# Kernel optimization log

Measured on AMD Instinct MI355X. Metric: run time of the kernel, lower is better.

The kernel has to match this reference:

```python
import jax, jax.numpy as jnp
import numpy as np

S, B, D = 2048, 2, 1024
H, HD = 16, 64  # head_num, head_dim
SCALE = 1.0 / (HD ** 0.5)


def setup_inputs() -> dict:
    key = jax.random.key(0)
    ks = jax.random.split(key, 7)
    std = 1.0 / np.sqrt(D)
    return {
        "inputs": jax.random.normal(ks[0], (S, B, D), dtype=jnp.float32),
        "Wkv": jax.random.uniform(ks[1], (D, 2 * H * HD), jnp.float32, -std, std),
        "bkv": jax.random.uniform(ks[2], (2 * H * HD,), jnp.float32, -std, std),
        "Wq": jax.random.uniform(ks[3], (D, H * HD), jnp.float32, -std, std),
        "bq": jax.random.uniform(ks[4], (H * HD,), jnp.float32, -std, std),
        "Wp": jax.random.uniform(ks[5], (H * HD, D), jnp.float32, -std, std),
        "bp": jax.random.uniform(ks[6], (D,), jnp.float32, -std, std),
    }


def reference(inputs, Wkv, bkv, Wq, bq, Wp, bp):
    s, b, _ = inputs.shape
    kv = inputs @ Wkv + bkv                      # [S,B,2*H*HD]
    k, v = jnp.split(kv, 2, axis=-1)
    q = inputs @ Wq + bq                         # [S,B,H*HD]
    k = k.reshape(s, b, H, HD)
    q = q.reshape(s, b, H, HD)
    v = v.reshape(s, b, H, HD)
    # scores: [B,H,S,S]
    attn = jnp.einsum("sbhd,tbhd->bhst", q, k) * SCALE
    attn = jax.nn.softmax(attn, axis=-1)         # dropout is identity in eval
    attn_vec = jnp.einsum("bhst,tbhd->sbhd", attn, v)
    attn_vec = attn_vec.reshape(s, b, H * HD)
    return attn_vec @ Wp + bp                    # [S,B,D]
```

## Files before the change

kernel.cpp:

```cpp
#include <hip/hip_runtime.h>
#include <hip/hip_bf16.h>
#include <stdint.h>


typedef __bf16 bf16_t;
typedef __bf16 bf16x8 __attribute__((ext_vector_type(8)));
typedef __bf16 bf16x4 __attribute__((ext_vector_type(4)));
typedef __bf16 bf16x2 __attribute__((ext_vector_type(2)));
typedef float f32x4 __attribute__((ext_vector_type(4)));
typedef float f32x16 __attribute__((ext_vector_type(16)));
typedef uint32_t u32;

#define S_LEN 2048
#define BATCH 2
#define DMODEL 1024
#define NHEAD 16
#define HDIM 64
#define KVB 64
#define FNT (S_LEN / KVB)
#define Q_SCALE 0.1803368801111204f

__device__ inline void gld16(const void* g, void* l)
{
    __builtin_amdgcn_global_load_lds(
        (const __attribute__((address_space(1))) void*)g,
        (__attribute__((address_space(3))) void*)l, 16, 0, 0);
}

__device__ inline u32 pack2(float a, float b)
{
    union { bf16x2 h; u32 u; } c;
    c.h[0] = (bf16_t)a; c.h[1] = (bf16_t)b;
    return c.u;
}

__global__ __launch_bounds__(256) void xcvt_kernel(
    const float* __restrict__ in, bf16_t* __restrict__ out)
{
    size_t i = ((size_t)blockIdx.x * 256 + threadIdx.x) * 8;
    float4 f0 = *(const float4*)(in + i);
    float4 f1 = *(const float4*)(in + i + 4);
    bf16x8 o;
    o[0] = (bf16_t)f0.x; o[1] = (bf16_t)f0.y; o[2] = (bf16_t)f0.z; o[3] = (bf16_t)f0.w;
    o[4] = (bf16_t)f1.x; o[5] = (bf16_t)f1.y; o[6] = (bf16_t)f1.z; o[7] = (bf16_t)f1.w;
    *(bf16x8*)(out + i) = o;
}

__global__ __launch_bounds__(256) void transpose_convert(
    const float* __restrict__ in, bf16_t* __restrict__ out, int K, int N)
{
    __shared__ float tile[64][65];
    int n0 = blockIdx.x * 64, k0 = blockIdx.y * 64;
    int r = threadIdx.x >> 2;
    int c = (threadIdx.x & 3) * 16;
    const float* src = in + (size_t)(k0 + r) * N + n0 + c;
#pragma unroll
    for (int j = 0; j < 16; j += 4) {
        float4 f = *(const float4*)(src + j);
        tile[r][c + j + 0] = f.x;
        tile[r][c + j + 1] = f.y;
        tile[r][c + j + 2] = f.z;
        tile[r][c + j + 3] = f.w;
    }
    __syncthreads();
    bf16x8 o0, o1;
#pragma unroll
    for (int j = 0; j < 8; ++j) o0[j] = (bf16_t)tile[c + j][r];
#pragma unroll
    for (int j = 0; j < 8; ++j) o1[j] = (bf16_t)tile[c + 8 + j][r];
    bf16_t* dst = out + (size_t)(n0 + r) * K + k0 + c;
    *(bf16x8*)dst = o0;
    *(bf16x8*)(dst + 8) = o1;
}

__global__ __launch_bounds__(256) void gemm_qkv(
    const bf16_t* __restrict__ A, const bf16_t* __restrict__ WT,
    const float* __restrict__ bkv, const float* __restrict__ bq,
    bf16_t* __restrict__ outK, bf16_t* __restrict__ outV,
    bf16_t* __restrict__ outQ)
{
    const int K = 1024;
    __shared__ __align__(16) char AsB[128 * 128];
    __shared__ __align__(16) char BsB[128 * 128];
    int tid = threadIdx.x;
    int wave = tid >> 6, lane = tid & 63;
    int l15 = lane & 15, l4 = lane >> 4;
    int m0 = blockIdx.x * 128, n0 = blockIdx.y * 128;
    int wr = (wave >> 1) * 64, wc = (wave & 1) * 64;

    char* ldsT = (wave < 2) ? AsB : BsB;
    const bf16_t* gbase = (wave < 2) ? A : WT;
    int rbase = (wave & 1) * 64;
    int tile0 = (wave < 2) ? m0 : n0;
    int srow = lane >> 3;
    int kcb = ((lane & 7) << 4) ^ (srow << 4);
    int rx = (l15 & 7) << 4;

    f32x4 acc[4][4] = {};

    for (int k0 = 0; k0 < K; k0 += 64) {
#pragma unroll
        for (int j = 0; j < 8; ++j) {
            const char* g = (const char*)(gbase +
                (size_t)(tile0 + rbase + j * 8 + srow) * K + k0) + kcb;
            gld16(g, ldsT + (rbase + j * 8) * 128);
        }
        __syncthreads();
#pragma unroll
        for (int kk = 0; kk < 2; ++kk) {
            int cb = (kk * 64 + l4 * 16) ^ rx;
            bf16x8 af[4], bfr[4];
#pragma unroll
            for (int i = 0; i < 4; ++i)
                af[i] = *(const bf16x8*)(AsB + (wr + i * 16 + l15) * 128 + cb);
#pragma unroll
            for (int i = 0; i < 4; ++i)
                bfr[i] = *(const bf16x8*)(BsB + (wc + i * 16 + l15) * 128 + cb);
#pragma unroll
            for (int mi = 0; mi < 4; ++mi)
#pragma unroll
                for (int ni = 0; ni < 4; ++ni)
                    acc[mi][ni] = __builtin_amdgcn_mfma_f32_16x16x32_bf16(
                        af[mi], bfr[ni], acc[mi][ni], 0, 0, 0);
        }
        __syncthreads();
    }

#pragma unroll
    for (int mi = 0; mi < 4; ++mi) {
#pragma unroll
        for (int ni = 0; ni < 4; ++ni) {
#pragma unroll
            for (int e = 0; e < 4; ++e) {
                int gm = m0 + wr + mi * 16 + l4 * 4 + e;
                int gn = n0 + wc + ni * 16 + l15;
                float bsel = (gn < 2048) ? bkv[gn] : bq[gn - 2048];
                float v = acc[mi][ni][e] + bsel;
                int s = gm >> 1, b = gm & 1;
                int nn = gn & 1023;
                int h = nn >> 6, d = nn & 63;
                size_t idx = ((size_t)((b << 4) + h) * S_LEN + s) * HDIM + d;
                if (gn < 1024)
                    outK[idx] = (bf16_t)v;
                else if (gn < 2048)
                    outV[idx] = (bf16_t)v;
                else
                    outQ[idx] = (bf16_t)(v * Q_SCALE);
            }
        }
    }
}

__global__ __launch_bounds__(256) void gemm_out_kernel(
    const bf16_t* __restrict__ A, const bf16_t* __restrict__ WT,
    const float* __restrict__ bias, float* __restrict__ outF)
{
    const int K = 1024, N = 1024;
    __shared__ __align__(16) char AsB[64 * 128];
    __shared__ __align__(16) char BsB[128 * 128];
    int tid = threadIdx.x, wave = tid >> 6, lane = tid & 63;
    int l15 = lane & 15, l4 = lane >> 4;
    int m0 = blockIdx.x * 64, n0 = blockIdx.y * 128;
    int wc = wave * 32;
    int srow = lane >> 3;
    int kcb = ((lane & 7) << 4) ^ (srow << 4);
    int rx = (l15 & 7) << 4;

    f32x4 acc[4][2] = {};

    for (int k0 = 0; k0 < K; k0 += 64) {
#pragma unroll
        for (int j = 0; j < 6; ++j) {
            int slot = wave * 6 + j;
            const bf16_t* g;
            char* l;
            if (slot < 8) {
                g = A + (size_t)(m0 + slot * 8 + srow) * K + k0;
                l = AsB + slot * 1024;
            } else {
                g = WT + (size_t)(n0 + (slot - 8) * 8 + srow) * K + k0;
                l = BsB + (slot - 8) * 1024;
            }
            gld16((const char*)g + kcb, l);
        }
        __syncthreads();
#pragma unroll
        for (int kk = 0; kk < 2; ++kk) {
            int cb = (kk * 64 + l4 * 16) ^ rx;
            bf16x8 af[4], bfr[2];
#pragma unroll
            for (int i = 0; i < 4; ++i)
                af[i] = *(const bf16x8*)(AsB + (i * 16 + l15) * 128 + cb);
#pragma unroll
            for (int i = 0; i < 2; ++i)
                bfr[i] = *(const bf16x8*)(BsB + (wc + i * 16 + l15) * 128 + cb);
#pragma unroll
            for (int mi = 0; mi < 4; ++mi)
#pragma unroll
                for (int ni = 0; ni < 2; ++ni)
                    acc[mi][ni] = __builtin_amdgcn_mfma_f32_16x16x32_bf16(
                        af[mi], bfr[ni], acc[mi][ni], 0, 0, 0);
        }
        __syncthreads();
    }

#pragma unroll
    for (int mi = 0; mi < 4; ++mi)
#pragma unroll
        for (int ni = 0; ni < 2; ++ni)
#pragma unroll
            for (int e = 0; e < 4; ++e) {
                int gm = m0 + mi * 16 + l4 * 4 + e;
                int gn = n0 + wc + ni * 16 + l15;
                outF[(size_t)gm * N + gn] = acc[mi][ni][e] + bias[gn];
            }
}

__global__ __launch_bounds__(256) void flash_kernel(
    const bf16_t* __restrict__ Qb, const bf16_t* __restrict__ Kb,
    const bf16_t* __restrict__ Vb, bf16_t* __restrict__ AVb)
{
    __shared__ __align__(16) char lds[34816];
    char* KsB = lds;
    bf16_t* VtB = (bf16_t*)(lds + 16384);

    int bh = blockIdx.y;
    int tid = threadIdx.x, wave = tid >> 6, lane = tid & 63;
    int l31 = lane & 31, hi = lane >> 5;

    const bf16_t* Qp = Qb + (size_t)bh * S_LEN * HDIM;
    const bf16_t* Kp = Kb + (size_t)bh * S_LEN * HDIM;
    const bf16_t* Vp = Vb + (size_t)bh * S_LEN * HDIM;

    int q0 = blockIdx.x * 128 + wave * 32;

    bf16x8 qf[4];
#pragma unroll
    for (int dc = 0; dc < 4; ++dc)
        qf[dc] = *(const bf16x8*)(Qp + (size_t)(q0 + l31) * HDIM + dc * 16 + hi * 8);

    f32x16 acc0 = {}, acc1 = {};
    float l_run = 0.f;

    int krow = lane >> 3;
    int kcb = ((lane & 7) << 4) ^ (krow << 4);
    int vd = (tid >> 4) * 4;
    int vt = (tid & 15) * 2;
    bf16x4 vreg[2][2];
    int swz = (l31 & 7) << 4;

#define STAGE_K(it, buf)                                                       \
    {                                                                          \
        _Pragma("unroll")                                                      \
        for (int j = 0; j < 2; ++j) {                                          \
            int t = wave * 16 + j * 8 + krow;                                  \
            const char* g = (const char*)Kp +                                  \
                ((size_t)((it) * KVB + t) * HDIM) * 2 + kcb;                   \
            gld16(g, KsB + (buf) * 8192 + (wave * 16 + j * 8) * 128);          \
        }                                                                      \
    }
#define LOAD_V(it)                                                             \
    {                                                                          \
        const bf16_t* vb = Vp + (size_t)((it) * KVB + vt) * HDIM + vd;         \
        vreg[0][0] = *(const bf16x4*)vb;                                       \
        vreg[0][1] = *(const bf16x4*)(vb + HDIM);                              \
        vreg[1][0] = *(const bf16x4*)(vb + 32 * HDIM);                         \
        vreg[1][1] = *(const bf16x4*)(vb + 33 * HDIM);                         \
    }
#define WRITE_V(buf)                                                           \
    {                                                                          \
        bf16_t* vtb = VtB + (buf) * 4608;                                      \
        _Pragma("unroll")                                                      \
        for (int p = 0; p < 2; ++p) {                                          \
            _Pragma("unroll")                                                  \
            for (int j = 0; j < 4; ++j) {                                      \
                bf16x2 w;                                                      \
                w[0] = vreg[p][0][j];                                          \
                w[1] = vreg[p][1][j];                                          \
                *(bf16x2*)&vtb[(vd + j) * 72 + vt + 32 * p] = w;               \
            }                                                                  \
        }                                                                      \
    }

    STAGE_K(0, 0);
    LOAD_V(0);
    WRITE_V(0);
    __syncthreads();

    for (int it = 0; it < FNT; ++it) {
        int cur = it & 1;
        if (it + 1 < FNT) {
            STAGE_K(it + 1, cur ^ 1);
            LOAD_V(it + 1);
        }

        f32x16 s0 = {}, s1 = {};
        __builtin_amdgcn_s_setprio(1);
#pragma unroll
        for (int dc = 0; dc < 4; ++dc) {
            bf16x8 k0 = *(const bf16x8*)(KsB + cur * 8192 + l31 * 128 +
                                         ((dc * 32 + hi * 16) ^ swz));
            bf16x8 k1 = *(const bf16x8*)(KsB + cur * 8192 + (32 + l31) * 128 +
                                         ((dc * 32 + hi * 16) ^ swz));
            s0 = __builtin_amdgcn_mfma_f32_32x32x16_bf16(k0, qf[dc], s0, 0, 0, 0);
            s1 = __builtin_amdgcn_mfma_f32_32x32x16_bf16(k1, qf[dc], s1, 0, 0, 0);
        }
        __builtin_amdgcn_s_setprio(0);

#pragma unroll
        for (int r = 0; r < 16; ++r) s0[r] = __builtin_amdgcn_exp2f(s0[r]);
#pragma unroll
        for (int r = 0; r < 16; ++r) s1[r] = __builtin_amdgcn_exp2f(s1[r]);
        float a8[8];
#pragma unroll
        for (int r = 0; r < 8; ++r)
            a8[r] = (s0[r] + s0[r + 8]) + (s1[r] + s1[r + 8]);
        float rs = ((a8[0] + a8[1]) + (a8[2] + a8[3])) +
                   ((a8[4] + a8[5]) + (a8[6] + a8[7]));
        rs += __shfl_xor(rs, 32);
        l_run += rs;

        __builtin_amdgcn_s_setprio(1);
#pragma unroll
        for (int s = 0; s < 4; ++s) {
            const int base = 8 * (s & 1);
            f32x16& P = (s < 2) ? s0 : s1;
            u32 a0 = pack2(P[base + 0], P[base + 1]);
            u32 a1 = pack2(P[base + 2], P[base + 3]);
            u32 b0 = pack2(P[base + 4], P[base + 5]);
            u32 b1 = pack2(P[base + 6], P[base + 7]);
            asm("v_permlane32_swap_b32 %0, %1" : "+v"(a0), "+v"(b0));
            asm("v_permlane32_swap_b32 %0, %1" : "+v"(a1), "+v"(b1));
            union { u32 u[4]; bf16x8 v; } pa;
            pa.u[0] = a0; pa.u[1] = a1; pa.u[2] = b0; pa.u[3] = b1;
            const bf16_t* vtb = VtB + cur * 4608;
            bf16x8 va0 = *(const bf16x8*)&vtb[l31 * 72 + s * 16 + hi * 8];
            bf16x8 va1 = *(const bf16x8*)&vtb[(32 + l31) * 72 + s * 16 + hi * 8];
            acc0 = __builtin_amdgcn_mfma_f32_32x32x16_bf16(va0, pa.v, acc0, 0, 0, 0);
            acc1 = __builtin_amdgcn_mfma_f32_32x32x16_bf16(va1, pa.v, acc1, 0, 0, 0);
        }
        __builtin_amdgcn_s_setprio(0);

        if (it + 1 < FNT) WRITE_V(cur ^ 1);
        __syncthreads();
    }

    bf16_t* sw = (bf16_t*)lds + wave * (32 * 72);
    float inv = 1.0f / l_run;
#pragma unroll
    for (int g = 0; g < 4; ++g) {
        bf16x4 w0, w1;
#pragma unroll
        for (int e = 0; e < 4; ++e) {
            w0[e] = (bf16_t)(acc0[4 * g + e] * inv);
            w1[e] = (bf16_t)(acc1[4 * g + e] * inv);
        }
        int d0 = 8 * g + 4 * hi;
        *(bf16x4*)&sw[l31 * 72 + d0] = w0;
        *(bf16x4*)&sw[l31 * 72 + 32 + d0] = w1;
    }
    __syncthreads();
    {
        int q = lane >> 1, half = lane & 1;
        const bf16_t* srow = sw + q * 72 + half * 32;
        int s = q0 + q;
        int b = bh >> 4, h = bh & 15;
        bf16_t* dst = AVb + ((size_t)s * BATCH + b) * DMODEL + h * HDIM + half * 32;
#pragma unroll
        for (int k = 0; k < 4; ++k)
            *(bf16x8*)(dst + k * 8) = *(const bf16x8*)(srow + k * 8);
    }
}

extern "C" void kernel_launch(void* const* d_in, const int* in_sizes, int n_in,
                              void* d_out, int out_size, void* d_ws, size_t ws_size,
                              hipStream_t stream)
{
    const float* X   = (const float*)d_in[0];
    const float* Wkv = (const float*)d_in[1];
    const float* bkv = (const float*)d_in[2];
    const float* Wq  = (const float*)d_in[3];
    const float* bq  = (const float*)d_in[4];
    const float* Wp  = (const float*)d_in[5];
    const float* bp  = (const float*)d_in[6];
    float* out = (float*)d_out;

    char* ws = (char*)d_ws;
    size_t off = 0;
    auto alloc = [&](size_t bytes) -> void* {
        void* p = ws + off;
        off += (bytes + 255) & ~(size_t)255;
        return p;
    };
    bf16_t* WqkvT = (bf16_t*)alloc((size_t)3072 * 1024 * 2);
    bf16_t* WpT   = (bf16_t*)alloc((size_t)1024 * 1024 * 2);
    bf16_t* Qb    = (bf16_t*)alloc((size_t)32 * S_LEN * HDIM * 2);
    bf16_t* Kb    = (bf16_t*)alloc((size_t)32 * S_LEN * HDIM * 2);
    bf16_t* Vb    = (bf16_t*)alloc((size_t)32 * S_LEN * HDIM * 2);
    bf16_t* Xbf   = (bf16_t*)alloc((size_t)4096 * 1024 * 2);
    bf16_t* AVb   = (bf16_t*)alloc((size_t)4096 * 1024 * 2);

    xcvt_kernel<<<2048, 256, 0, stream>>>(X, Xbf);
    transpose_convert<<<dim3(32, 16), 256, 0, stream>>>(Wkv, WqkvT, 1024, 2048);
    transpose_convert<<<dim3(16, 16), 256, 0, stream>>>(
        Wq, WqkvT + (size_t)2048 * 1024, 1024, 1024);
    transpose_convert<<<dim3(16, 16), 256, 0, stream>>>(Wp, WpT, 1024, 1024);

    gemm_qkv<<<dim3(32, 24), 256, 0, stream>>>(Xbf, WqkvT, bkv, bq, Kb, Vb, Qb);
    flash_kernel<<<dim3(S_LEN / 128, 32), 256, 0, stream>>>(Qb, Kb, Vb, AVb);
    gemm_out_kernel<<<dim3(64, 8), 256, 0, stream>>>(AVb, WpT, bp, out);
}
```

Before: 128.9 us.

## Split flash attention KV range in two with a separate reduce kernel, fuse prep kernels

```diff
diff --git a/kernel.cpp b/kernel.cpp
--- a/kernel.cpp
+++ b/kernel.cpp
@@ -17,7 +17,7 @@
 #define NHEAD 16
 #define HDIM 64
 #define KVB 64
-#define FNT (S_LEN / KVB)
+#define HITER 16
 #define Q_SCALE 0.1803368801111204f
 
 __device__ inline void gld16(const void* g, void* l)
@@ -34,23 +34,43 @@
     return c.u;
 }
 
-__global__ __launch_bounds__(256) void xcvt_kernel(
-    const float* __restrict__ in, bf16_t* __restrict__ out)
-{
-    size_t i = ((size_t)blockIdx.x * 256 + threadIdx.x) * 8;
-    float4 f0 = *(const float4*)(in + i);
-    float4 f1 = *(const float4*)(in + i + 4);
-    bf16x8 o;
-    o[0] = (bf16_t)f0.x; o[1] = (bf16_t)f0.y; o[2] = (bf16_t)f0.z; o[3] = (bf16_t)f0.w;
-    o[4] = (bf16_t)f1.x; o[5] = (bf16_t)f1.y; o[6] = (bf16_t)f1.z; o[7] = (bf16_t)f1.w;
-    *(bf16x8*)(out + i) = o;
-}
-
-__global__ __launch_bounds__(256) void transpose_convert(
-    const float* __restrict__ in, bf16_t* __restrict__ out, int K, int N)
+__global__ __launch_bounds__(256) void prep_kernel(
+    const float* __restrict__ X, bf16_t* __restrict__ Xbf,
+    const float* __restrict__ Wkv, const float* __restrict__ Wq,
+    const float* __restrict__ Wp, bf16_t* __restrict__ WqkvT,
+    bf16_t* __restrict__ WpT)
 {
     __shared__ float tile[64][65];
-    int n0 = blockIdx.x * 64, k0 = blockIdx.y * 64;
+    int bid = blockIdx.x;
+    if (bid < 2048) {
+        size_t i = ((size_t)bid * 256 + threadIdx.x) * 8;
+        float4 f0 = *(const float4*)(X + i);
+        float4 f1 = *(const float4*)(X + i + 4);
+        bf16x8 o;
+        o[0] = (bf16_t)f0.x; o[1] = (bf16_t)f0.y;
+        o[2] = (bf16_t)f0.z; o[3] = (bf16_t)f0.w;
+        o[4] = (bf16_t)f1.x; o[5] = (bf16_t)f1.y;
+        o[6] = (bf16_t)f1.z; o[7] = (bf16_t)f1.w;
+        *(bf16x8*)(Xbf + i) = o;
+        return;
+    }
+    const float* in;
+    bf16_t* out;
+    int N, n0, k0;
+    const int K = 1024;
+    if (bid < 2560) {
+        int id = bid - 2048;
+        in = Wkv; out = WqkvT; N = 2048;
+        n0 = (id & 31) * 64; k0 = (id >> 5) * 64;
+    } else if (bid < 2816) {
+        int id = bid - 2560;
+        in = Wq; out = WqkvT + (size_t)2048 * 1024; N = 1024;
+        n0 = (id & 15) * 64; k0 = (id >> 4) * 64;
+    } else {
+        int id = bid - 2816;
+        in = Wp; out = WpT; N = 1024;
+        n0 = (id & 15) * 64; k0 = (id >> 4) * 64;
+    }
     int r = threadIdx.x >> 2;
     int c = (threadIdx.x & 3) * 16;
     const float* src = in + (size_t)(k0 + r) * N + n0 + c;
@@ -218,13 +238,19 @@
 
 __global__ __launch_bounds__(256) void flash_kernel(
     const bf16_t* __restrict__ Qb, const bf16_t* __restrict__ Kb,
-    const bf16_t* __restrict__ Vb, bf16_t* __restrict__ AVb)
+    const bf16_t* __restrict__ Vb, float* __restrict__ Opart,
+    float* __restrict__ Lpart)
 {
     __shared__ __align__(16) char lds[34816];
     char* KsB = lds;
     bf16_t* VtB = (bf16_t*)(lds + 16384);
 
-    int bh = blockIdx.y;
+    int bid = blockIdx.x;
+    int id = (bid & 7) * 128 + (bid >> 3);
+    int bh = id >> 5;
+    int qx = (id >> 1) & 15;
+    int half = id & 1;
+
     int tid = threadIdx.x, wave = tid >> 6, lane = tid & 63;
     int l31 = lane & 31, hi = lane >> 5;
 
@@ -232,7 +258,7 @@
     const bf16_t* Kp = Kb + (size_t)bh * S_LEN * HDIM;
     const bf16_t* Vp = Vb + (size_t)bh * S_LEN * HDIM;
 
-    int q0 = blockIdx.x * 128 + wave * 32;
+    int q0 = qx * 128 + wave * 32;
 
     bf16x8 qf[4];
 #pragma unroll
@@ -282,14 +308,15 @@
         }                                                                      \
     }
 
-    STAGE_K(0, 0);
-    LOAD_V(0);
+    STAGE_K(half * HITER, 0);
+    LOAD_V(half * HITER);
     WRITE_V(0);
     __syncthreads();
 
-    for (int it = 0; it < FNT; ++it) {
-        int cur = it & 1;
-        if (it + 1 < FNT) {
+    for (int i = 0; i < HITER; ++i) {
+        int cur = i & 1;
+        int it = half * HITER + i;
+        if (i + 1 < HITER) {
             STAGE_K(it + 1, cur ^ 1);
             LOAD_V(it + 1);
         }
@@ -341,19 +368,52 @@
         }
         __builtin_amdgcn_s_setprio(0);
 
-        if (it + 1 < FNT) WRITE_V(cur ^ 1);
+        if (i + 1 < HITER) WRITE_V(cur ^ 1);
         __syncthreads();
     }
 
-    bf16_t* sw = (bf16_t*)lds + wave * (32 * 72);
-    float inv = 1.0f / l_run;
+    int T = (bh * 16 + qx) * 4 + wave;
+    float* op = Opart + ((size_t)T * 2 + half) * 2048;
 #pragma unroll
     for (int g = 0; g < 4; ++g) {
+        f32x4 w0, w1;
+#pragma unroll
+        for (int e = 0; e < 4; ++e) { w0[e] = acc0[4 * g + e]; w1[e] = acc1[4 * g + e]; }
+        *(f32x4*)(op + g * 256 + lane * 4) = w0;
+        *(f32x4*)(op + (g + 4) * 256 + lane * 4) = w1;
+    }
+    if (lane < 32) Lpart[((size_t)T * 2 + half) * 32 + lane] = l_run;
+}
+
+__global__ __launch_bounds__(256) void reduce_kernel(
+    const float* __restrict__ Opart, const float* __restrict__ Lpart,
+    bf16_t* __restrict__ AVb)
+{
+    __shared__ bf16_t sw_all[4][32 * 72];
+    int tid = threadIdx.x, wave = tid >> 6, lane = tid & 63;
+    int l31 = lane & 31, hi = lane >> 5;
+    int T = blockIdx.x * 4 + wave;
+    int bh = T >> 6, qx = (T >> 2) & 15, wv = T & 3;
+    int q0 = qx * 128 + wv * 32;
+
+    const float* o0 = Opart + (size_t)T * 2 * 2048;
+    const float* o1 = o0 + 2048;
+    float lsum = Lpart[(size_t)T * 2 * 32 + l31] +
+                 Lpart[((size_t)T * 2 + 1) * 32 + l31];
+    float inv = 1.0f / lsum;
+
+    bf16_t* sw = sw_all[wave];
+#pragma unroll
+    for (int g = 0; g < 4; ++g) {
+        f32x4 a0 = *(const f32x4*)(o0 + g * 256 + lane * 4);
+        f32x4 b0 = *(const f32x4*)(o1 + g * 256 + lane * 4);
+        f32x4 a1 = *(const f32x4*)(o0 + (g + 4) * 256 + lane * 4);
+        f32x4 b1 = *(const f32x4*)(o1 + (g + 4) * 256 + lane * 4);
         bf16x4 w0, w1;
 #pragma unroll
         for (int e = 0; e < 4; ++e) {
-            w0[e] = (bf16_t)(acc0[4 * g + e] * inv);
-            w1[e] = (bf16_t)(acc1[4 * g + e] * inv);
+            w0[e] = (bf16_t)((a0[e] + b0[e]) * inv);
+            w1[e] = (bf16_t)((a1[e] + b1[e]) * inv);
         }
         int d0 = 8 * g + 4 * hi;
         *(bf16x4*)&sw[l31 * 72 + d0] = w0;
@@ -361,11 +421,11 @@
     }
     __syncthreads();
     {
-        int q = lane >> 1, half = lane & 1;
-        const bf16_t* srow = sw + q * 72 + half * 32;
+        int q = lane >> 1, hf = lane & 1;
+        const bf16_t* srow = sw + q * 72 + hf * 32;
         int s = q0 + q;
         int b = bh >> 4, h = bh & 15;
-        bf16_t* dst = AVb + ((size_t)s * BATCH + b) * DMODEL + h * HDIM + half * 32;
+        bf16_t* dst = AVb + ((size_t)s * BATCH + b) * DMODEL + h * HDIM + hf * 32;
 #pragma unroll
         for (int k = 0; k < 4; ++k)
             *(bf16x8*)(dst + k * 8) = *(const bf16x8*)(srow + k * 8);
@@ -397,16 +457,14 @@
     bf16_t* Qb    = (bf16_t*)alloc((size_t)32 * S_LEN * HDIM * 2);
     bf16_t* Kb    = (bf16_t*)alloc((size_t)32 * S_LEN * HDIM * 2);
     bf16_t* Vb    = (bf16_t*)alloc((size_t)32 * S_LEN * HDIM * 2);
-    bf16_t* Xbf   = (bf16_t*)alloc((size_t)4096 * 1024 * 2);
     bf16_t* AVb   = (bf16_t*)alloc((size_t)4096 * 1024 * 2);
-
-    xcvt_kernel<<<2048, 256, 0, stream>>>(X, Xbf);
-    transpose_convert<<<dim3(32, 16), 256, 0, stream>>>(Wkv, WqkvT, 1024, 2048);
-    transpose_convert<<<dim3(16, 16), 256, 0, stream>>>(
-        Wq, WqkvT + (size_t)2048 * 1024, 1024, 1024);
-    transpose_convert<<<dim3(16, 16), 256, 0, stream>>>(Wp, WpT, 1024, 1024);
-
+    float*  Opart = (float*)alloc((size_t)2048 * 2 * 2048 * 4);
+    float*  Lpart = (float*)alloc((size_t)2048 * 2 * 32 * 4);
+    bf16_t* Xbf   = (bf16_t*)Opart;
+
+    prep_kernel<<<3072, 256, 0, stream>>>(X, Xbf, Wkv, Wq, Wp, WqkvT, WpT);
     gemm_qkv<<<dim3(32, 24), 256, 0, stream>>>(Xbf, WqkvT, bkv, bq, Kb, Vb, Qb);
-    flash_kernel<<<dim3(S_LEN / 128, 32), 256, 0, stream>>>(Qb, Kb, Vb, AVb);
+    flash_kernel<<<1024, 256, 0, stream>>>(Qb, Kb, Vb, Opart, Lpart);
+    reduce_kernel<<<512, 256, 0, stream>>>(Opart, Lpart, AVb);
     gemm_out_kernel<<<dim3(64, 8), 256, 0, stream>>>(AVb, WpT, bp, out);
 }
```

New measurement: 133.3 us. +3.5%, slower.
